# Kernel tuning notes

Hardware: AMD Instinct MI355X
Metric: run time of the kernel (lower is better)

## Reference

```python
import jax, jax.numpy as jnp
import numpy as np

N, E, D, NUM_REL, NUM_LAYERS = 20000, 100000, 768, 7, 5  # 6 edge types + self-loop relation


def setup_inputs() -> dict:
    key = jax.random.key(0)
    ks = jax.random.split(key, 8)
    x = jax.random.normal(ks[0], (N, D), dtype=jnp.float32)
    edge_index = jax.random.randint(ks[1], (2, E), 0, N, dtype=jnp.int64)
    # original edge_type values are in [-1, 5]; module adds 1 -> [0, 6]
    edge_type = jax.random.randint(ks[2], (E,), -1, 6, dtype=jnp.int64)
    scale = 1.0 / np.sqrt(D)
    weights = jax.random.normal(ks[3], (NUM_LAYERS, NUM_REL, D, D), dtype=jnp.float32) * scale
    roots = jax.random.normal(ks[4], (NUM_LAYERS, D, D), dtype=jnp.float32) * scale
    biases = jax.random.normal(ks[5], (NUM_LAYERS, D), dtype=jnp.float32) * 0.01
    return {"x": x, "edge_index": edge_index, "edge_type": edge_type,
            "weights": weights, "roots": roots, "biases": biases}


def _rgcn_conv(h, src, dst, safe_et, W, root, b):
    # PyG RGCNConv (aggr='mean', root_weight=True, bias=True):
    #   out = x @ root + b + sum_r mean_{edges of rel r into v}(x[src]) @ W_r
    n = h.shape[0]
    hs = h[src]  # [E, D] gather once, reused across relations
    out = h @ root + b
    for r in range(NUM_REL):
        m = (safe_et == r).astype(h.dtype)  # [E]
        msg_sum = jax.ops.segment_sum(hs * m[:, None], dst, num_segments=n)  # [N, D]
        cnt = jax.ops.segment_sum(m, dst, num_segments=n)  # [N]
        mean = msg_sum / jnp.maximum(cnt, 1.0)[:, None]  # zero where no rel-r edges
        out = out + mean @ W[r]
    return out


def reference(x, edge_index, edge_type, weights, roots, biases):
    src, dst = edge_index[0], edge_index[1]
    safe_et = edge_type + 1  # [-1..5] -> [0..6]
    h = x
    for l in range(NUM_LAYERS):
        h = _rgcn_conv(h, src, dst, safe_et, weights[l], roots[l], biases[l])
        h = jax.nn.relu(h)  # dropout=0 -> identity
    return h
```

## Files before the change

### kernel.cpp

```cpp
#include <hip/hip_runtime.h>

typedef unsigned short u16;
typedef unsigned int   u32;
typedef __attribute__((ext_vector_type(8))) short short8;
typedef __attribute__((ext_vector_type(4))) float f32x4;

#define DD      768
#define KK      6144
#define NREL    7
#define NLAYERS 5

__device__ __forceinline__ float b2f(u16 v) {
  return __uint_as_float(((u32)v) << 16);
}
__device__ __forceinline__ u16 f2bf(float f) {
  u32 x = __float_as_uint(f);
  x += 0x7fffu + ((x >> 16) & 1u);
  return (u16)(x >> 16);
}
__device__ __forceinline__ void gload16(const void* g, void* l) {
  __builtin_amdgcn_global_load_lds(
      (const __attribute__((address_space(1))) void*)g,
      (__attribute__((address_space(3))) void*)l, 16, 0, 0);
}


__global__ void cast_x_kernel(const float* __restrict__ x, u16* __restrict__ H, size_t n) {
  for (size_t i = ((size_t)blockIdx.x * 256 + threadIdx.x) * 4; i < n; i += (size_t)gridDim.x * 256 * 4) {
    float4 v = *(const float4*)&x[i];
    u32 lo = (u32)f2bf(v.x) | ((u32)f2bf(v.y) << 16);
    u32 hi = (u32)f2bf(v.z) | ((u32)f2bf(v.w) << 16);
    uint2 o; o.x = lo; o.y = hi;
    *(uint2*)&H[i] = o;
  }
}

__global__ void count_kernel(const int* __restrict__ eidx, const int* __restrict__ etype,
                             int* cnt_dst, int* cnt_rel, int E, int Nn) {
  int e = blockIdx.x * 256 + threadIdx.x;
  if (e >= E) return;
  int dst = eidx[E + e];
  int rel = etype[e] + 1;
  atomicAdd(&cnt_dst[dst], 1);
  atomicAdd(&cnt_rel[(size_t)rel * Nn + dst], 1);
}

__global__ __launch_bounds__(1024) void scan_kernel(const int* __restrict__ cnt, int* __restrict__ offs, int n) {
  __shared__ int part[1024];
  int t = threadIdx.x;
  int per = (n + 1023) / 1024;
  int base = t * per;
  int s = 0;
  for (int i = 0; i < per; ++i) { int idx = base + i; if (idx < n) s += cnt[idx]; }
  part[t] = s;
  __syncthreads();
  for (int o = 1; o < 1024; o <<= 1) {
    int v = (t >= o) ? part[t - o] : 0;
    __syncthreads();
    part[t] += v;
    __syncthreads();
  }
  int excl = (t == 0) ? 0 : part[t - 1];
  s = excl;
  for (int i = 0; i < per; ++i) { int idx = base + i; if (idx < n) { offs[idx] = s; s += cnt[idx]; } }
  if (t == 1023) offs[n] = part[1023];
}

__global__ void fillperm_kernel(const int* __restrict__ eidx, const int* __restrict__ offs,
                                int* fill, int* perm, int E) {
  int e = blockIdx.x * 256 + threadIdx.x;
  if (e >= E) return;
  int dst = eidx[E + e];
  int pos = offs[dst] + atomicAdd(&fill[dst], 1);
  perm[pos] = e;
}

__global__ void wcat_kernel(const float* __restrict__ W, const float* __restrict__ R, u16* __restrict__ Bt) {
  __shared__ float t[32 * 33];
  int b = blockIdx.x;
  int s = b / 576, rem = b % 576;
  int kt = rem / 24, nt = rem % 24;
  const float* src = (s == 0) ? R : (W + (size_t)(s - 1) * DD * DD);
  int tj = threadIdx.x & 31, ti = threadIdx.x >> 5;
#pragma unroll
  for (int i = 0; i < 4; ++i) {
    int kk = kt * 32 + ti + i * 8;
    t[(ti + i * 8) * 33 + tj] = src[(size_t)kk * DD + nt * 32 + tj];
  }
  __syncthreads();
#pragma unroll
  for (int i = 0; i < 4; ++i) {
    int nn_ = nt * 32 + ti + i * 8;
    Bt[(size_t)nn_ * KK + (size_t)s * DD + kt * 32 + tj] = f2bf(t[tj * 33 + ti + i * 8]);
  }
}

__global__ void copy_h_kernel(const u16* __restrict__ Hin, u16* __restrict__ Acat, int nn) {
  size_t total = (size_t)nn * (DD / 8);
  for (size_t i = (size_t)blockIdx.x * 256 + threadIdx.x; i < total; i += (size_t)gridDim.x * 256) {
    size_t r = i / (DD / 8), c = i % (DD / 8);
    *(uint4*)&Acat[r * KK + c * 8] = *(const uint4*)&Hin[r * DD + c * 8];
  }
}

__global__ __launch_bounds__(192) void aggregate_kernel(
    const u16* __restrict__ H, const int* __restrict__ esrc, const int* __restrict__ etype,
    const int* __restrict__ offs, const int* __restrict__ perm, const int* __restrict__ cnt_rel,
    u16* __restrict__ Acat, int node0, int Nn) {
  int v = node0 + blockIdx.x;
  int t = threadIdx.x;
  int j0 = t * 4;
  float a0[4] = {0,0,0,0}, a1[4] = {0,0,0,0}, a2[4] = {0,0,0,0}, a3[4] = {0,0,0,0};
  float a4[4] = {0,0,0,0}, a5[4] = {0,0,0,0}, a6[4] = {0,0,0,0};
  int beg = offs[v], end = offs[v + 1];
  for (int e = beg; e < end; ++e) {
    int eid = perm[e];
    int src = esrc[eid];
    int rel = etype[eid] + 1;
    uint2 w = *(const uint2*)&H[(size_t)src * DD + j0];
    float f0 = b2f((u16)(w.x & 0xffff));
    float f1 = b2f((u16)(w.x >> 16));
    float f2 = b2f((u16)(w.y & 0xffff));
    float f3 = b2f((u16)(w.y >> 16));
    switch (rel) {
      case 0: a0[0]+=f0; a0[1]+=f1; a0[2]+=f2; a0[3]+=f3; break;
      case 1: a1[0]+=f0; a1[1]+=f1; a1[2]+=f2; a1[3]+=f3; break;
      case 2: a2[0]+=f0; a2[1]+=f1; a2[2]+=f2; a2[3]+=f3; break;
      case 3: a3[0]+=f0; a3[1]+=f1; a3[2]+=f2; a3[3]+=f3; break;
      case 4: a4[0]+=f0; a4[1]+=f1; a4[2]+=f2; a4[3]+=f3; break;
      case 5: a5[0]+=f0; a5[1]+=f1; a5[2]+=f2; a5[3]+=f3; break;
      default: a6[0]+=f0; a6[1]+=f1; a6[2]+=f2; a6[3]+=f3; break;
    }
  }
  size_t rowbase = (size_t)blockIdx.x * KK;
  const float* regs[NREL] = {a0, a1, a2, a3, a4, a5, a6};
#pragma unroll
  for (int r = 0; r < NREL; ++r) {
    int c = cnt_rel[(size_t)r * Nn + v];
    float inv = (c > 0) ? 1.f / (float)c : 0.f;
    const float* a = regs[r];
    u32 lo = (u32)f2bf(a[0] * inv) | ((u32)f2bf(a[1] * inv) << 16);
    u32 hi = (u32)f2bf(a[2] * inv) | ((u32)f2bf(a[3] * inv) << 16);
    uint2 o; o.x = lo; o.y = hi;
    *(uint2*)&Acat[rowbase + (size_t)(r + 1) * DD + j0] = o;
  }
}


__global__ __launch_bounds__(512, 2) void gemm256_kernel(
    const u16* __restrict__ A, const u16* __restrict__ Bt, const float* __restrict__ bias,
    u16* __restrict__ Hout, float* __restrict__ Cout, int Mvalid, int Mtiles) {
  __shared__ u16 sm[4][16384];

  int tid = threadIdx.x;
  int lane = tid & 63;
  int wv = tid >> 6;
  int wm = wv >> 2, wn = wv & 3;

  int nwg = Mtiles * 3;
  int orig = (int)blockIdx.x;
  int q8 = nwg >> 3, r8 = nwg & 7;
  int xcd = orig & 7, rank = orig >> 3;
  int wg = (xcd < r8 ? xcd * (q8 + 1) : r8 * (q8 + 1) + (xcd - r8) * q8) + rank;
  int bm = wg / 3, bn = wg % 3;

  const char* gA[2];
  const char* gB[2];
#pragma unroll
  for (int j = 0; j < 2; ++j) {
    int qq = j * 8192 + tid * 16;
    int qp = qq ^ (((qq >> 9) & 1) << 5);
    int row = ((qp >> 10) << 4) | ((qp >> 6) & 15);
    int kb  = qp & 63;
    gA[j] = (const char*)A  + (size_t)(bm * 256 + row) * (KK * 2) + kb;
    gB[j] = (const char*)Bt + (size_t)(bn * 256 + row) * (KK * 2) + kb;
  }
  int rsel = lane & 15;
  int laneoff = ((rsel * 64) + ((lane >> 4) * 16)) ^ ((rsel & 8) << 2);

  f32x4 acc[8][4];
#pragma unroll
  for (int m = 0; m < 8; ++m)
#pragma unroll
    for (int n = 0; n < 4; ++n) acc[m][n] = (f32x4){0.f, 0.f, 0.f, 0.f};

  const int NSTEP = KK / 32;

#define STAGE(t2)                                                        \
  do {                                                                   \
    int s_ = (t2) & 3;                                                   \
    size_t ko_ = (size_t)(t2) * 64;                                      \
    char* d_ = (char*)&sm[s_][0];                                        \
    gload16(gA[0] + ko_, d_ + tid * 16);                                 \
    gload16(gA[1] + ko_, d_ + 8192 + tid * 16);                          \
    gload16(gB[0] + ko_, d_ + 16384 + tid * 16);                         \
    gload16(gB[1] + ko_, d_ + 16384 + 8192 + tid * 16);                  \
  } while (0)

#define READF(t2, ar, br)                                                \
  do {                                                                   \
    const char* base_ = (const char*)&sm[(t2) & 3][0];                   \
    _Pragma("unroll")                                                    \
    for (int m = 0; m < 8; ++m)                                          \
      ar[m] = *(const short8*)(base_ + (wm * 8 + m) * 1024 + laneoff);   \
    _Pragma("unroll")                                                    \
    for (int n = 0; n < 4; ++n)                                          \
      br[n] = *(const short8*)(base_ + 16384 + (wn * 4 + n) * 1024 + laneoff); \
  } while (0)

#define MFMA32(ar, br)                                                   \
  do {                                                                   \
    _Pragma("unroll")                                                    \
    for (int m = 0; m < 8; ++m)                                          \
      _Pragma("unroll")                                                  \
      for (int n = 0; n < 4; ++n)                                        \
        acc[m][n] = __builtin_amdgcn_mfma_f32_16x16x32_bf16(ar[m], br[n], acc[m][n], 0, 0, 0); \
  } while (0)

  short8 aE[8], bE[4], aO[8], bO[4];

  STAGE(0); STAGE(1); STAGE(2);
  asm volatile("s_waitcnt vmcnt(4)" ::: "memory");
  __builtin_amdgcn_s_barrier();
  __builtin_amdgcn_sched_barrier(0);
  READF(0, aE, bE);

  for (int t = 0; t < NSTEP; t += 2) {
    if (t + 3 < NSTEP) STAGE(t + 3);
    READF(t + 1, aO, bO);
    __builtin_amdgcn_sched_barrier(0);
    __builtin_amdgcn_s_setprio(1);
    MFMA32(aE, bE);
    __builtin_amdgcn_s_setprio(0);
    asm volatile("s_waitcnt vmcnt(4)" ::: "memory");
    __builtin_amdgcn_s_barrier();
    __builtin_amdgcn_sched_barrier(0);

    if (t + 4 < NSTEP) STAGE(t + 4);
    if (t + 2 < NSTEP) READF(t + 2, aE, bE);
    __builtin_amdgcn_sched_barrier(0);
    __builtin_amdgcn_s_setprio(1);
    MFMA32(aO, bO);
    __builtin_amdgcn_s_setprio(0);
    asm volatile("s_waitcnt vmcnt(4)" ::: "memory");
    __builtin_amdgcn_s_barrier();
    __builtin_amdgcn_sched_barrier(0);
  }
#undef STAGE
#undef READF
#undef MFMA32

  int rif = (lane >> 4) * 4;
  int cidx = lane & 15;
#pragma unroll
  for (int m = 0; m < 8; ++m) {
    int rl = bm * 256 + wm * 128 + m * 16 + rif;
#pragma unroll
    for (int n = 0; n < 4; ++n) {
      int c = bn * 256 + wn * 64 + n * 16 + cidx;
      float bv = bias[c];
#pragma unroll
      for (int j = 0; j < 4; ++j) {
        int r = rl + j;
        if (r < Mvalid) {
          float v = acc[m][n][j] + bv;
          v = v > 0.f ? v : 0.f;
          if (Hout) Hout[(size_t)r * DD + c] = f2bf(v);
          if (Cout) Cout[(size_t)r * DD + c] = v;
        }
      }
    }
  }
}


static inline size_t alignup(size_t x, size_t a) { return (x + a - 1) & ~(a - 1); }

extern "C" void kernel_launch(void* const* d_in, const int* in_sizes, int n_in,
                              void* d_out, int out_size, void* d_ws, size_t ws_size,
                              hipStream_t stream) {
  const float* x       = (const float*)d_in[0];
  const int*   eidx    = (const int*)d_in[1];
  const int*   etype   = (const int*)d_in[2];
  const float* weights = (const float*)d_in[3];
  const float* roots   = (const float*)d_in[4];
  const float* biases  = (const float*)d_in[5];
  float* out = (float*)d_out;

  const int Nn = in_sizes[0] / DD;
  const int E  = in_sizes[2];

  char* p = (char*)d_ws;
  size_t off = 0;
  auto carve = [&](size_t bytes) -> char* {
    char* r = p + off;
    off = alignup(off + bytes, 256);
    return r;
  };
  u16* H0      = (u16*)carve((size_t)Nn * DD * 2);
  u16* Bt      = (u16*)carve((size_t)DD * KK * 2);
  int* cnt_rel = (int*)carve((size_t)NREL * Nn * 4);
  int* cnt_dst = (int*)carve((size_t)Nn * 4);
  int* offs    = (int*)carve((size_t)(Nn + 1) * 4);
  int* fill    = (int*)carve((size_t)Nn * 4);
  int* perm    = (int*)carve((size_t)E * 4);

  size_t rem = (ws_size > off) ? (ws_size - off) : 0;
  int McCap = (int)(rem / ((size_t)KK * 2));
  int Mpad = ((Nn + 255) / 256) * 256;
  int Mc = (McCap < Mpad) ? (McCap & ~255) : Mpad;
  if (Mc < 256) return;
  u16* Acat = (u16*)(p + off);
  int nchunks = (Nn + Mc - 1) / Mc;
  u16* H1 = (u16*)d_out;

  (void)hipMemsetAsync(cnt_rel, 0, (size_t)NREL * Nn * 4, stream);
  (void)hipMemsetAsync(cnt_dst, 0, (size_t)Nn * 4, stream);
  (void)hipMemsetAsync(fill, 0, (size_t)Nn * 4, stream);

  int eg = (E + 255) / 256;
  count_kernel<<<eg, 256, 0, stream>>>(eidx, etype, cnt_dst, cnt_rel, E, Nn);
  scan_kernel<<<1, 1024, 0, stream>>>(cnt_dst, offs, Nn);
  fillperm_kernel<<<eg, 256, 0, stream>>>(eidx, offs, fill, perm, E);
  cast_x_kernel<<<2048, 256, 0, stream>>>(x, H0, (size_t)Nn * DD);

  const u16* Hin = H0;
  u16* Hnext = H1;
  for (int l = 0; l < NLAYERS; ++l) {
    wcat_kernel<<<8 * 576, 256, 0, stream>>>(weights + (size_t)l * NREL * DD * DD,
                                             roots + (size_t)l * DD * DD, Bt);
    for (int c = 0; c < nchunks; ++c) {
      int node0 = c * Mc;
      int nn = (Nn - node0 < Mc) ? (Nn - node0) : Mc;
      int copy16 = nn * (DD / 8);
      int cb = (copy16 + 255) / 256;
      if (cb > 2048) cb = 2048;
      copy_h_kernel<<<cb, 256, 0, stream>>>(Hin + (size_t)node0 * DD, Acat, nn);
      aggregate_kernel<<<nn, 192, 0, stream>>>(Hin, eidx, etype, offs, perm, cnt_rel,
                                               Acat, node0, Nn);
      int mt = (nn + 255) / 256;
      u16* ho = (l < NLAYERS - 1) ? (Hnext + (size_t)node0 * DD) : nullptr;
      float* co = (l == NLAYERS - 1) ? (out + (size_t)node0 * DD) : nullptr;
      gemm256_kernel<<<mt * 3, 512, 0, stream>>>(Acat, Bt, biases + (size_t)l * DD, ho, co, nn, mt);
    }
    const u16* t_ = Hin;
    Hin = Hnext;
    Hnext = (u16*)t_;
  }
}
```

Baseline: 1.482 ms.

## Fold self-row copy into aggregate and restructure GEMM to 64-wide K double buffer

The separate copy_h kernel is removed and each aggregate block now copies its own node's H row into the root slot of Acat, saving one launch and one pass per chunk. The GEMM main loop moves from a 4-stage, 32-wide K pipeline to a 2-stage double buffer with 64-wide K tiles, using an XOR-swizzled 128-byte row layout. Each K step is split into four MFMA quadrants, with LDS fragment reads and next-tile global loads interleaved between them. This cuts the register held for fragments but adds more barriers per step and a shallower prefetch depth, which may expose more global-load latency.

```diff
diff --git a/kernel.cpp b/kernel.cpp
--- a/kernel.cpp
+++ b/kernel.cpp
@@ -95,14 +95,6 @@
   }
 }
 
-__global__ void copy_h_kernel(const u16* __restrict__ Hin, u16* __restrict__ Acat, int nn) {
-  size_t total = (size_t)nn * (DD / 8);
-  for (size_t i = (size_t)blockIdx.x * 256 + threadIdx.x; i < total; i += (size_t)gridDim.x * 256) {
-    size_t r = i / (DD / 8), c = i % (DD / 8);
-    *(uint4*)&Acat[r * KK + c * 8] = *(const uint4*)&Hin[r * DD + c * 8];
-  }
-}
-
 __global__ __launch_bounds__(192) void aggregate_kernel(
     const u16* __restrict__ H, const int* __restrict__ esrc, const int* __restrict__ etype,
     const int* __restrict__ offs, const int* __restrict__ perm, const int* __restrict__ cnt_rel,
@@ -110,6 +102,8 @@
   int v = node0 + blockIdx.x;
   int t = threadIdx.x;
   int j0 = t * 4;
+  size_t rowbase = (size_t)blockIdx.x * KK;
+  *(uint2*)&Acat[rowbase + j0] = *(const uint2*)&H[(size_t)v * DD + j0];
   float a0[4] = {0,0,0,0}, a1[4] = {0,0,0,0}, a2[4] = {0,0,0,0}, a3[4] = {0,0,0,0};
   float a4[4] = {0,0,0,0}, a5[4] = {0,0,0,0}, a6[4] = {0,0,0,0};
   int beg = offs[v], end = offs[v + 1];
@@ -132,7 +126,6 @@
       default: a6[0]+=f0; a6[1]+=f1; a6[2]+=f2; a6[3]+=f3; break;
     }
   }
-  size_t rowbase = (size_t)blockIdx.x * KK;
   const float* regs[NREL] = {a0, a1, a2, a3, a4, a5, a6};
 #pragma unroll
   for (int r = 0; r < NREL; ++r) {
@@ -147,10 +140,12 @@
 }
 
 
+#define MFMA_(a_, b_, c_) __builtin_amdgcn_mfma_f32_16x16x32_bf16(a_, b_, c_, 0, 0, 0)
+
 __global__ __launch_bounds__(512, 2) void gemm256_kernel(
     const u16* __restrict__ A, const u16* __restrict__ Bt, const float* __restrict__ bias,
     u16* __restrict__ Hout, float* __restrict__ Cout, int Mvalid, int Mtiles) {
-  __shared__ u16 sm[4][16384];
+  __shared__ u16 sm[2][2][16384];
 
   int tid = threadIdx.x;
   int lane = tid & 63;
@@ -164,19 +159,15 @@
   int wg = (xcd < r8 ? xcd * (q8 + 1) : r8 * (q8 + 1) + (xcd - r8) * q8) + rank;
   int bm = wg / 3, bn = wg % 3;
 
-  const char* gA[2];
-  const char* gB[2];
-#pragma unroll
-  for (int j = 0; j < 2; ++j) {
-    int qq = j * 8192 + tid * 16;
-    int qp = qq ^ (((qq >> 9) & 1) << 5);
-    int row = ((qp >> 10) << 4) | ((qp >> 6) & 15);
-    int kb  = qp & 63;
-    gA[j] = (const char*)A  + (size_t)(bm * 256 + row) * (KK * 2) + kb;
-    gB[j] = (const char*)Bt + (size_t)(bn * 256 + row) * (KK * 2) + kb;
-  }
-  int rsel = lane & 15;
-  int laneoff = ((rsel * 64) + ((lane >> 4) * 16)) ^ ((rsel & 8) << 2);
+  int srow = tid >> 3;
+  int sc = (tid & 7) ^ (srow & 7);
+  const char* gA0 = (const char*)A  + (size_t)(bm * 256 + srow) * (KK * 2) + sc * 16;
+  const char* gB0 = (const char*)Bt + (size_t)(bn * 256 + srow) * (KK * 2) + sc * 16;
+  const size_t JSTRIDE = (size_t)64 * KK * 2;
+
+  int rsel = lane & 15, kq = lane >> 4;
+  int off0 = rsel * 128 + (((kq)     ^ (rsel & 7)) * 16);
+  int off1 = rsel * 128 + (((kq + 4) ^ (rsel & 7)) * 16);
 
   f32x4 acc[8][4];
 #pragma unroll
@@ -184,71 +175,115 @@
 #pragma unroll
     for (int n = 0; n < 4; ++n) acc[m][n] = (f32x4){0.f, 0.f, 0.f, 0.f};
 
-  const int NSTEP = KK / 32;
-
-#define STAGE(t2)                                                        \
-  do {                                                                   \
-    int s_ = (t2) & 3;                                                   \
-    size_t ko_ = (size_t)(t2) * 64;                                      \
-    char* d_ = (char*)&sm[s_][0];                                        \
-    gload16(gA[0] + ko_, d_ + tid * 16);                                 \
-    gload16(gA[1] + ko_, d_ + 8192 + tid * 16);                          \
-    gload16(gB[0] + ko_, d_ + 16384 + tid * 16);                         \
-    gload16(gB[1] + ko_, d_ + 16384 + 8192 + tid * 16);                  \
-  } while (0)
-
-#define READF(t2, ar, br)                                                \
-  do {                                                                   \
-    const char* base_ = (const char*)&sm[(t2) & 3][0];                   \
-    _Pragma("unroll")                                                    \
-    for (int m = 0; m < 8; ++m)                                          \
-      ar[m] = *(const short8*)(base_ + (wm * 8 + m) * 1024 + laneoff);   \
-    _Pragma("unroll")                                                    \
-    for (int n = 0; n < 4; ++n)                                          \
-      br[n] = *(const short8*)(base_ + 16384 + (wn * 4 + n) * 1024 + laneoff); \
-  } while (0)
-
-#define MFMA32(ar, br)                                                   \
-  do {                                                                   \
-    _Pragma("unroll")                                                    \
-    for (int m = 0; m < 8; ++m)                                          \
-      _Pragma("unroll")                                                  \
-      for (int n = 0; n < 4; ++n)                                        \
-        acc[m][n] = __builtin_amdgcn_mfma_f32_16x16x32_bf16(ar[m], br[n], acc[m][n], 0, 0, 0); \
-  } while (0)
-
-  short8 aE[8], bE[4], aO[8], bO[4];
-
-  STAGE(0); STAGE(1); STAGE(2);
-  asm volatile("s_waitcnt vmcnt(4)" ::: "memory");
+  const int NKT = KK / 64;
+
+#pragma unroll
+  for (int j = 0; j < 4; ++j)
+    gload16(gA0 + (size_t)j * JSTRIDE, (char*)&sm[0][0][0] + j * 8192 + tid * 16);
+#pragma unroll
+  for (int j = 0; j < 4; ++j)
+    gload16(gB0 + (size_t)j * JSTRIDE, (char*)&sm[0][1][0] + j * 8192 + tid * 16);
+  asm volatile("s_waitcnt vmcnt(0)" ::: "memory");
   __builtin_amdgcn_s_barrier();
   __builtin_amdgcn_sched_barrier(0);
-  READF(0, aE, bE);
-
-  for (int t = 0; t < NSTEP; t += 2) {
-    if (t + 3 < NSTEP) STAGE(t + 3);
-    READF(t + 1, aO, bO);
+
+  for (int t = 0; t < NKT; ++t) {
+    int s = t & 1;
+    const char* aB = (const char*)&sm[s][0][0];
+    const char* bB = (const char*)&sm[s][1][0];
+    char* aN = (char*)&sm[s ^ 1][0][0];
+    char* bN = (char*)&sm[s ^ 1][1][0];
+    size_t ko = (size_t)(t + 1) * 128;
+    int more = (t + 1 < NKT);
+
+    short8 a03[4][2], a47[4][2], bb[2][2];
+
+#pragma unroll
+    for (int m = 0; m < 4; ++m) {
+      a03[m][0] = *(const short8*)(aB + (wm * 128 + m * 16) * 128 + off0);
+      a03[m][1] = *(const short8*)(aB + (wm * 128 + m * 16) * 128 + off1);
+    }
+#pragma unroll
+    for (int n = 0; n < 2; ++n) {
+      bb[n][0] = *(const short8*)(bB + (wn * 64 + n * 16) * 128 + off0);
+      bb[n][1] = *(const short8*)(bB + (wn * 64 + n * 16) * 128 + off1);
+    }
+    if (more) {
+#pragma unroll
+      for (int j = 0; j < 4; ++j)
+        gload16(gA0 + (size_t)j * JSTRIDE + ko, aN + j * 8192 + tid * 16);
+    }
+    asm volatile("s_waitcnt lgkmcnt(8)" ::: "memory");
+    __builtin_amdgcn_s_barrier();
+    asm volatile("s_waitcnt lgkmcnt(0)" ::: "memory");
     __builtin_amdgcn_sched_barrier(0);
     __builtin_amdgcn_s_setprio(1);
-    MFMA32(aE, bE);
+#pragma unroll
+    for (int m = 0; m < 4; ++m)
+#pragma unroll
+      for (int n = 0; n < 2; ++n) {
+        acc[m][n] = MFMA_(a03[m][0], bb[n][0], acc[m][n]);
+        acc[m][n] = MFMA_(a03[m][1], bb[n][1], acc[m][n]);
+      }
     __builtin_amdgcn_s_setprio(0);
-    asm volatile("s_waitcnt vmcnt(4)" ::: "memory");
-    __builtin_amdgcn_s_barrier();
-    __builtin_amdgcn_sched_barrier(0);
-
-    if (t + 4 < NSTEP) STAGE(t + 4);
-    if (t + 2 < NSTEP) READF(t + 2, aE, bE);
+    __builtin_amdgcn_s_barrier();
+
+#pragma unroll
+    for (int m = 0; m < 4; ++m) {
+      a47[m][0] = *(const short8*)(aB + (wm * 128 + (m + 4) * 16) * 128 + off0);
+      a47[m][1] = *(const short8*)(aB + (wm * 128 + (m + 4) * 16) * 128 + off1);
+    }
+    if (more) {
+#pragma unroll
+      for (int j = 0; j < 4; ++j)
+        gload16(gB0 + (size_t)j * JSTRIDE + ko, bN + j * 8192 + tid * 16);
+    }
+    __builtin_amdgcn_s_barrier();
+    asm volatile("s_waitcnt lgkmcnt(0)" ::: "memory");
     __builtin_amdgcn_sched_barrier(0);
     __builtin_amdgcn_s_setprio(1);
-    MFMA32(aO, bO);
+#pragma unroll
+    for (int m = 0; m < 4; ++m)
+#pragma unroll
+      for (int n = 0; n < 2; ++n) {
+        acc[m + 4][n] = MFMA_(a47[m][0], bb[n][0], acc[m + 4][n]);
+        acc[m + 4][n] = MFMA_(a47[m][1], bb[n][1], acc[m + 4][n]);
+      }
     __builtin_amdgcn_s_setprio(0);
-    asm volatile("s_waitcnt vmcnt(4)" ::: "memory");
-    __builtin_amdgcn_s_barrier();
+    __builtin_amdgcn_s_barrier();
+
+#pragma unroll
+    for (int n = 0; n < 2; ++n) {
+      bb[n][0] = *(const short8*)(bB + (wn * 64 + (n + 2) * 16) * 128 + off0);
+      bb[n][1] = *(const short8*)(bB + (wn * 64 + (n + 2) * 16) * 128 + off1);
+    }
+    __builtin_amdgcn_s_barrier();
+    asm volatile("s_waitcnt lgkmcnt(0)" ::: "memory");
     __builtin_amdgcn_sched_barrier(0);
-  }
-#undef STAGE
-#undef READF
-#undef MFMA32
+    __builtin_amdgcn_s_setprio(1);
+#pragma unroll
+    for (int m = 0; m < 4; ++m)
+#pragma unroll
+      for (int n = 0; n < 2; ++n) {
+        acc[m + 4][n + 2] = MFMA_(a47[m][0], bb[n][0], acc[m + 4][n + 2]);
+        acc[m + 4][n + 2] = MFMA_(a47[m][1], bb[n][1], acc[m + 4][n + 2]);
+      }
+    __builtin_amdgcn_s_setprio(0);
+    __builtin_amdgcn_s_barrier();
+
+    __builtin_amdgcn_s_setprio(1);
+#pragma unroll
+    for (int m = 0; m < 4; ++m)
+#pragma unroll
+      for (int n = 0; n < 2; ++n) {
+        acc[m][n + 2] = MFMA_(a03[m][0], bb[n][0], acc[m][n + 2]);
+        acc[m][n + 2] = MFMA_(a03[m][1], bb[n][1], acc[m][n + 2]);
+      }
+    __builtin_amdgcn_s_setprio(0);
+    asm volatile("s_waitcnt vmcnt(0)" ::: "memory");
+    __builtin_amdgcn_s_barrier();
+    __builtin_amdgcn_sched_barrier(0);
+  }
 
   int rif = (lane >> 4) * 4;
   int cidx = lane & 15;
@@ -332,10 +367,6 @@
     for (int c = 0; c < nchunks; ++c) {
       int node0 = c * Mc;
       int nn = (Nn - node0 < Mc) ? (Nn - node0) : Mc;
-      int copy16 = nn * (DD / 8);
-      int cb = (copy16 + 255) / 256;
-      if (cb > 2048) cb = 2048;
-      copy_h_kernel<<<cb, 256, 0, stream>>>(Hin + (size_t)node0 * DD, Acat, nn);
       aggregate_kernel<<<nn, 192, 0, stream>>>(Hin, eidx, etype, offs, perm, cnt_rel,
                                                Acat, node0, Nn);
       int mt = (nn + 255) / 256;
```

Result: no change. 1.481 ms (-0.1%).
